# Kernel optimization log

Measured on AMD Instinct MI355X. Metric: run time of the kernel, lower is better.

The kernel has to match this reference:

```python
import jax, jax.numpy as jnp
import numpy as np

EMBED = 512
HEADS = 8
HEAD_DIM = EMBED // HEADS
EPS = 1e-5


def setup_inputs() -> dict:
    key = jax.random.key(0)
    ks = jax.random.split(key, 10)
    s = 1.0 / np.sqrt(EMBED)
    x = jax.random.normal(ks[0], (2, 4096, EMBED), dtype=jnp.float32)
    Wq = jax.random.uniform(ks[1], (EMBED, EMBED), jnp.float32, -s, s)
    bq = jnp.zeros((EMBED,), jnp.float32)
    Wk = jax.random.uniform(ks[2], (EMBED, EMBED), jnp.float32, -s, s)
    bk = jnp.zeros((EMBED,), jnp.float32)
    Wv = jax.random.uniform(ks[3], (EMBED, EMBED), jnp.float32, -s, s)
    bv = jnp.zeros((EMBED,), jnp.float32)
    Wo = jax.random.uniform(ks[4], (EMBED, EMBED), jnp.float32, -s, s)
    bo = jnp.zeros((EMBED,), jnp.float32)
    gamma = jnp.ones((EMBED,), jnp.float32)
    beta = jnp.zeros((EMBED,), jnp.float32)
    return {"x": x, "Wq": Wq, "bq": bq, "Wk": Wk, "bk": bk,
            "Wv": Wv, "bv": bv, "Wo": Wo, "bo": bo,
            "gamma": gamma, "beta": beta}


def reference(x, Wq, bq, Wk, bk, Wv, bv, Wo, bo, gamma, beta):
    b, n, e = x.shape
    def split_heads(t):  # [b,n,e] -> [b,h,n,d]
        return t.reshape(b, n, HEADS, HEAD_DIM).transpose(0, 2, 1, 3)
    q = split_heads(x @ Wq + bq)
    k = split_heads(x @ Wk + bk)
    v = split_heads(x @ Wv + bv)
    energy = jnp.einsum('bhqd,bhkd->bhqk', q, k) * (HEAD_DIM ** -0.5)
    attn = jax.nn.softmax(energy, axis=-1)  # dropout=0.0 (eval)
    out = jnp.einsum('bhqk,bhkd->bhqd', attn, v)
    out = out.transpose(0, 2, 1, 3).reshape(b, n, e)
    out = out @ Wo + bo
    y = x + out
    mu = jnp.mean(y, axis=-1, keepdims=True)
    var = jnp.var(y, axis=-1, keepdims=True)
    return (y - mu) * jax.lax.rsqrt(var + EPS) * gamma + beta
```

## Files before the change

### kernel.cpp

```cpp
#include <hip/hip_runtime.h>
#include <hip/hip_bf16.h>


#define ROWS 8192
#define EMB  512
#define SEQ  4096
#define HEADS 8
#define HD   64
#define QSCALE 0.18033688011112042f

typedef __attribute__((ext_vector_type(8))) short bf16x8;
typedef __attribute__((ext_vector_type(4))) short bf16x4;
typedef __attribute__((ext_vector_type(4))) float f32x4;

__device__ __forceinline__ float bf16_to_f(unsigned short u) {
    union { unsigned int i; float f; } v; v.i = ((unsigned int)u) << 16; return v.f;
}
__device__ __forceinline__ unsigned short f_to_bf16(float f) {
    union { __hip_bfloat16 h; unsigned short u; } v; v.h = __float2bfloat16(f); return v.u;
}
__device__ __forceinline__ unsigned int pack_bf16_trunc(float a, float b) {
    return __builtin_amdgcn_perm(__float_as_uint(b), __float_as_uint(a), 0x07060302u);
}
__device__ __forceinline__ void load_lds16(const void* g, void* l) {
    __builtin_amdgcn_global_load_lds(
        (const __attribute__((address_space(1))) void*)g,
        (__attribute__((address_space(3))) void*)l, 16, 0, 0);
}

__device__ __forceinline__ int detect_fp32(const void* x) {
    const unsigned short* p = (const unsigned short*)x;
    int t = threadIdx.x & 63;
    int cnt = 0;
    #pragma unroll
    for (int i = 0; i < 4; ++i) {
        unsigned short u = p[t * 4 + i];
        int e = (u >> 7) & 0xFF;
        cnt += (e >= 140) ? 1 : 0;
    }
    #pragma unroll
    for (int off = 32; off > 0; off >>= 1) cnt += __shfl_xor(cnt, off, 64);
    return cnt > 16;
}

__global__ __launch_bounds__(256) void prep_kernel(
        const void* __restrict__ x, unsigned short* __restrict__ xb,
        const void* W0, const void* W1, const void* W2, const void* W3,
        unsigned short* __restrict__ Wt,
        const void* b0, const void* b1, const void* b2, const void* b3,
        const void* b4, const void* b5, float* __restrict__ bias_all) {
    int fp32 = detect_fp32(x);
    int bid = blockIdx.x;
    int tid = threadIdx.x;
    if (bid < 4096) {
        if (!fp32) return;
        int i = (bid * 256 + tid) * 4;
        float4 v = *(const float4*)((const float*)x + i);
        ushort4 u = { f_to_bf16(v.x), f_to_bf16(v.y), f_to_bf16(v.z), f_to_bf16(v.w) };
        *(ushort4*)(xb + i) = u;
    } else if (bid < 4352) {
        __shared__ float T[64][65];
        int idx0 = bid - 4096;
        int kt = idx0 & 7, nt = (idx0 >> 3) & 7, mat = idx0 >> 6;
        const void* src = (mat == 0) ? W0 : (mat == 1) ? W1 : (mat == 2) ? W2 : W3;
        for (int ii = 0; ii < 4; ++ii) {
            int idx = tid + ii * 256;
            int i = idx >> 4, j = (idx & 15) * 4;
            size_t g = (size_t)(kt * 64 + i) * 512 + nt * 64 + j;
            if (fp32) {
                float4 v = *(const float4*)((const float*)src + g);
                T[i][j] = v.x; T[i][j+1] = v.y; T[i][j+2] = v.z; T[i][j+3] = v.w;
            } else {
                ushort4 u = *(const ushort4*)((const unsigned short*)src + g);
                T[i][j] = bf16_to_f(u.x); T[i][j+1] = bf16_to_f(u.y);
                T[i][j+2] = bf16_to_f(u.z); T[i][j+3] = bf16_to_f(u.w);
            }
        }
        __syncthreads();
        for (int ii = 0; ii < 2; ++ii) {
            int idx = tid + ii * 256;
            int j = idx >> 3, ch = idx & 7;
            unsigned short pk[8];
            for (int t = 0; t < 8; ++t) pk[t] = f_to_bf16(T[ch * 8 + t][j]);
            *(bf16x8*)&Wt[(size_t)(mat * 512 + nt * 64 + j) * 512 + kt * 64 + ch * 8] = *(bf16x8*)pk;
        }
    } else {
        int idx = (bid - 4352) * 256 + tid;
        int mat = idx >> 9, off = idx & 511;
        const void* src = (mat == 0) ? b0 : (mat == 1) ? b1 : (mat == 2) ? b2 :
                          (mat == 3) ? b3 : (mat == 4) ? b4 : b5;
        float v;
        if (fp32) v = ((const float*)src)[off];
        else      v = bf16_to_f(((const unsigned short*)src)[off]);
        bias_all[idx] = v;
    }
}

template <typename OutT>
__global__ __launch_bounds__(256) void gemm_mfma_kernel(
        const unsigned short* __restrict__ A_conv, const unsigned short* __restrict__ A_raw,
        const unsigned short* __restrict__ Bt,
        const float* __restrict__ bias, OutT* __restrict__ C, int ldc, int scale_cols,
        unsigned short* __restrict__ VtOut) {
    __shared__ __align__(16) unsigned short smemg[2][2][128 * 64];
    const unsigned short* A = detect_fp32(A_raw) ? A_conv : A_raw;
    int tid = threadIdx.x;
    int wave = tid >> 6, lane = tid & 63;
    int l15 = lane & 15, quad = lane >> 4;

    int lin = blockIdx.x + gridDim.x * blockIdx.y;
    int nwg = gridDim.x * gridDim.y;
    int bx, by;
    if (nwg & 7) { bx = blockIdx.x; by = blockIdx.y; }
    else {
        int t = (lin & 7) * (nwg >> 3) + (lin >> 3);
        bx = t % gridDim.x; by = t / gridDim.x;
    }
    int m0 = by * 128, n0 = bx * 128;
    int wm = (wave & 1) * 64, wn = (wave >> 1) * 64;
    bool is_v = (VtOut != nullptr) && (n0 >= 1024);

    int rt = wave * 32 + (lane >> 3);
    int ch = (lane & 7) ^ ((lane >> 3) & 7);
    const unsigned short* ag = A  + (size_t)(m0 + rt) * 512 + ch * 8;
    const unsigned short* bg = Bt + (size_t)(n0 + rt) * 512 + ch * 8;

    f32x4 acc[4][4];
    for (int i = 0; i < 4; ++i) for (int j = 0; j < 4; ++j) acc[i][j] = (f32x4){0.f,0.f,0.f,0.f};

#define GSTAGE(buf, k0) do {                                                      \
        unsigned short* Atb = &smemg[buf][0][0];                                  \
        unsigned short* Bsb = &smemg[buf][1][0];                                  \
        _Pragma("unroll")                                                         \
        for (int j = 0; j < 4; ++j) {                                             \
            load_lds16(ag + (size_t)(j * 8) * 512 + (k0), &Atb[(wave * 32 + j * 8) * 64]); \
            load_lds16(bg + (size_t)(j * 8) * 512 + (k0), &Bsb[(wave * 32 + j * 8) * 64]); \
        }                                                                         \
    } while (0)

    GSTAGE(0, 0);

    for (int s = 0; s < 8; ++s) {
        int cur = s & 1;
        asm volatile("s_waitcnt vmcnt(0)" ::: "memory");
        __builtin_amdgcn_sched_barrier(0);
        asm volatile("s_barrier" ::: "memory");
        __builtin_amdgcn_sched_barrier(0);
        if (s + 1 < 8) GSTAGE(cur ^ 1, (s + 1) * 64);

        const unsigned short* At = &smemg[cur][0][0];
        const unsigned short* Bs = &smemg[cur][1][0];
        #pragma unroll
        for (int ks = 0; ks < 2; ++ks) {
            bf16x8 a[4], b[4];
            #pragma unroll
            for (int f = 0; f < 4; ++f) {
                int pc = ((ks * 4 + quad) ^ (l15 & 7)) * 8;
                a[f] = *(const bf16x8*)&At[(wm + f * 16 + l15) * 64 + pc];
                b[f] = *(const bf16x8*)&Bs[(wn + f * 16 + l15) * 64 + pc];
            }
            if (is_v) {
                #pragma unroll
                for (int fm = 0; fm < 4; ++fm)
                    #pragma unroll
                    for (int fn = 0; fn < 4; ++fn)
                        acc[fm][fn] = __builtin_amdgcn_mfma_f32_16x16x32_bf16(a[fm], b[fn], acc[fm][fn], 0, 0, 0);
            } else {
                #pragma unroll
                for (int fm = 0; fm < 4; ++fm)
                    #pragma unroll
                    for (int fn = 0; fn < 4; ++fn)
                        acc[fm][fn] = __builtin_amdgcn_mfma_f32_16x16x32_bf16(b[fn], a[fm], acc[fm][fn], 0, 0, 0);
            }
        }
        __builtin_amdgcn_sched_barrier(0);
    }
#undef GSTAGE

    __syncthreads();
    unsigned short* LT = &smemg[0][0][0];

    float sc = (n0 < scale_cols) ? QSCALE : 1.f;

    if (is_v) {
        #pragma unroll
        for (int fm = 0; fm < 4; ++fm) {
            #pragma unroll
            for (int fn = 0; fn < 4; ++fn) {
                int dcol = wn + fn * 16 + l15;
                float bia = bias[n0 + dcol];
                int seq0 = wm + fm * 16 + quad * 4;
                ushort4 pk = { f_to_bf16(acc[fm][fn][0] + bia),
                               f_to_bf16(acc[fm][fn][1] + bia),
                               f_to_bf16(acc[fm][fn][2] + bia),
                               f_to_bf16(acc[fm][fn][3] + bia) };
                int c8 = (seq0 >> 2) ^ (dcol & 31);
                *(ushort4*)&LT[dcol * 128 + c8 * 4] = pk;
            }
        }
    } else {
        #pragma unroll
        for (int fm = 0; fm < 4; ++fm) {
            #pragma unroll
            for (int fn = 0; fn < 4; ++fn) {
                int row = wm + fm * 16 + l15;
                int col0 = wn + fn * 16 + quad * 4;
                float4 b4 = *(const float4*)&bias[n0 + col0];
                ushort4 pk = { f_to_bf16((acc[fm][fn][0] + b4.x) * sc),
                               f_to_bf16((acc[fm][fn][1] + b4.y) * sc),
                               f_to_bf16((acc[fm][fn][2] + b4.z) * sc),
                               f_to_bf16((acc[fm][fn][3] + b4.w) * sc) };
                int c8 = (col0 >> 2) ^ (row & 31);
                *(ushort4*)&LT[row * 128 + c8 * 4] = pk;
            }
        }
    }
    __syncthreads();
    #pragma unroll
    for (int i = 0; i < 16; ++i) {
        int row = wave * 32 + i * 2 + (lane >> 5);
        int c8 = lane & 31;
        int phys = c8 ^ (row & 31);
        ushort4 v4 = *(const ushort4*)&LT[row * 128 + phys * 4];
        if (is_v) {
            int hd = n0 - 1024 + row;
            int bh = (m0 >> 12) * 8 + (hd >> 6);
            int d  = hd & 63;
            *(ushort4*)&VtOut[((size_t)(bh * 64 + d)) * SEQ + (m0 & 4095) + c8 * 4] = v4;
        } else {
            *(ushort4*)&C[(size_t)(m0 + row) * ldc + n0 + c8 * 4] = v4;
        }
    }
}

__global__ __launch_bounds__(256, 4) void attn_kernel(
        const unsigned short* __restrict__ QKV, const unsigned short* __restrict__ Vt,
        unsigned short* __restrict__ Ab) {
    __shared__ __align__(16) unsigned char smem[32768];
    float* Ored = (float*)smem;
    float* Lred = (float*)(smem + 16384);

    int tid = threadIdx.x;
    int wave = tid >> 6, lane = tid & 63;
    int l15 = lane & 15, quad = lane >> 4;
    int qh = wave >> 1, kh = wave & 1;
    int lin = blockIdx.x;
    int xcd = lin & 7, slot = lin >> 3;
    int grp = xcd + 8 * (slot >> 6);
    int qt = slot & 63;
    int h = grp & 7, b = grp >> 3;
    int bh = b * HEADS + h;
    size_t qrow0 = (size_t)b * SEQ + qt * 64;

    bf16x8 aq[2][2];
    #pragma unroll
    for (int t = 0; t < 2; ++t) {
        const unsigned short* qp = &QKV[(qrow0 + qh * 32 + t * 16 + l15) * 1536 + h * 64];
        aq[t][0] = *(const bf16x8*)&qp[quad * 8];
        aq[t][1] = *(const bf16x8*)&qp[32 + quad * 8];
    }
    f32x4 o[2][4];
    #pragma unroll
    for (int t = 0; t < 2; ++t)
        #pragma unroll
        for (int db = 0; db < 4; ++db) o[t][db] = (f32x4){0.f, 0.f, 0.f, 0.f};
    float lp[2] = {0.f, 0.f};

    int r8 = lane >> 3;
    int kch = (lane & 7) ^ (r8 & 7);
    int r0 = wave * 16 + r8;
    int r1 = wave * 16 + 8 + r8;
    int p0r = (r0 & 32) | (((r0 >> 2) & 3) << 3) | (((r0 >> 4) & 1) << 2) | (r0 & 3);
    int p1r = (r1 & 32) | (((r1 >> 2) & 3) << 3) | (((r1 >> 4) & 1) << 2) | (r1 & 3);
    const unsigned short* kg0 = &QKV[((size_t)b * SEQ + p0r) * 1536 + 512 + h * 64 + kch * 8];
    const unsigned short* kg1 = &QKV[((size_t)b * SEQ + p1r) * 1536 + 512 + h * 64 + kch * 8];
    const unsigned short* vg = &Vt[((size_t)bh * 64 + wave * 16 + r8) * SEQ + kch * 8];

#define STAGE(buf, kt2) do {                                                          \
        unsigned short* Ksb = (unsigned short*)(smem + (buf) * 8192);                 \
        unsigned short* Vsb = (unsigned short*)(smem + 16384 + (buf) * 8192);         \
        load_lds16(kg0 + (size_t)((kt2) * 64) * 1536, &Ksb[(wave * 16) * 64]);        \
        load_lds16(kg1 + (size_t)((kt2) * 64) * 1536, &Ksb[(wave * 16 + 8) * 64]);    \
        load_lds16(vg + (size_t)((kt2) * 64), &Vsb[(wave * 16) * 64]);                \
        load_lds16(vg + (size_t)((kt2) * 64) + (size_t)8 * SEQ,                       \
                   &Vsb[(wave * 16 + 8) * 64]);                                       \
    } while (0)

    STAGE(0, 0);

    for (int kt = 0; kt < SEQ / 64; ++kt) {
        int cur = kt & 1;
        asm volatile("s_waitcnt vmcnt(0)" ::: "memory");
        __builtin_amdgcn_sched_barrier(0);
        asm volatile("s_barrier" ::: "memory");
        __builtin_amdgcn_sched_barrier(0);
        if (kt + 1 < SEQ / 64) STAGE(cur ^ 1, kt + 1);

        const unsigned short* Ksc = (const unsigned short*)(smem + cur * 8192);
        const unsigned short* Vsc = (const unsigned short*)(smem + 16384 + cur * 8192);

        bf16x8 kA[2][2];
        #pragma unroll
        for (int nb = 0; nb < 2; ++nb) {
            int krow = kh * 32 + nb * 16 + l15;
            int key = krow & 7;
            kA[nb][0] = *(const bf16x8*)&Ksc[krow * 64 + (quad ^ key) * 8];
            kA[nb][1] = *(const bf16x8*)&Ksc[krow * 64 + ((4 + quad) ^ key) * 8];
        }
        bf16x8 bv8[4];
        #pragma unroll
        for (int db = 0; db < 4; ++db) {
            int d = db * 16 + l15;
            bv8[db] = *(const bf16x8*)&Vsc[d * 64 + (((kh * 4 + quad) ^ (d & 7))) * 8];
        }
        #pragma unroll
        for (int t = 0; t < 2; ++t) {
            f32x4 sv0 = {0.f, 0.f, 0.f, 0.f};
            f32x4 sv1 = {0.f, 0.f, 0.f, 0.f};
            __builtin_amdgcn_s_setprio(1);
            sv0 = __builtin_amdgcn_mfma_f32_16x16x32_bf16(kA[0][0], aq[t][0], sv0, 0, 0, 0);
            sv0 = __builtin_amdgcn_mfma_f32_16x16x32_bf16(kA[0][1], aq[t][1], sv0, 0, 0, 0);
            sv1 = __builtin_amdgcn_mfma_f32_16x16x32_bf16(kA[1][0], aq[t][0], sv1, 0, 0, 0);
            sv1 = __builtin_amdgcn_mfma_f32_16x16x32_bf16(kA[1][1], aq[t][1], sv1, 0, 0, 0);
            __builtin_amdgcn_s_setprio(0);
            float p0 = __builtin_amdgcn_exp2f(sv0[0]);
            float p1 = __builtin_amdgcn_exp2f(sv0[1]);
            float p2 = __builtin_amdgcn_exp2f(sv0[2]);
            float p3 = __builtin_amdgcn_exp2f(sv0[3]);
            float p4 = __builtin_amdgcn_exp2f(sv1[0]);
            float p5 = __builtin_amdgcn_exp2f(sv1[1]);
            float p6 = __builtin_amdgcn_exp2f(sv1[2]);
            float p7 = __builtin_amdgcn_exp2f(sv1[3]);
            lp[t] += ((p0 + p1) + (p2 + p3)) + ((p4 + p5) + (p6 + p7));
            union { unsigned int u[4]; bf16x8 v; } ap;
            ap.u[0] = pack_bf16_trunc(p0, p1);
            ap.u[1] = pack_bf16_trunc(p2, p3);
            ap.u[2] = pack_bf16_trunc(p4, p5);
            ap.u[3] = pack_bf16_trunc(p6, p7);
            __builtin_amdgcn_s_setprio(1);
            #pragma unroll
            for (int db = 0; db < 4; ++db)
                o[t][db] = __builtin_amdgcn_mfma_f32_16x16x32_bf16(ap.v, bv8[db], o[t][db], 0, 0, 0);
            __builtin_amdgcn_s_setprio(0);
        }
        __builtin_amdgcn_sched_barrier(0);
    }
#undef STAGE

    __syncthreads();
    #pragma unroll
    for (int t = 0; t < 2; ++t) {
        float v = lp[t];
        v += __shfl_xor(v, 16, 64);
        v += __shfl_xor(v, 32, 64);
        if (quad == 0) Lred[(wave * 2 + t) * 16 + l15] = v;
    }
    __syncthreads();
    float* myO = Ored + wave * (16 * 64);
    #pragma unroll
    for (int t = 0; t < 2; ++t) {
        #pragma unroll
        for (int db = 0; db < 4; ++db)
            #pragma unroll
            for (int r = 0; r < 4; ++r)
                myO[(quad * 4 + r) * 64 + db * 16 + l15] = o[t][db][r];
        __syncthreads();
        {
            int q_l = tid >> 3;
            int dg = tid & 7;
            int qh2 = q_l >> 4, qq = q_l & 15;
            const float* r0p = Ored + (qh2 * 2 + 0) * (16 * 64) + qq * 64 + dg * 8;
            const float* r1p = Ored + (qh2 * 2 + 1) * (16 * 64) + qq * 64 + dg * 8;
            float4 a0 = *(const float4*)&r0p[0];
            float4 a1 = *(const float4*)&r0p[4];
            float4 c0 = *(const float4*)&r1p[0];
            float4 c1 = *(const float4*)&r1p[4];
            float lt = Lred[((qh2 * 2 + 0) * 2 + t) * 16 + qq] +
                       Lred[((qh2 * 2 + 1) * 2 + t) * 16 + qq];
            float inv = 1.f / lt;
            size_t row = qrow0 + qh2 * 32 + t * 16 + qq;
            unsigned short* dst = &Ab[row * EMB + h * 64 + dg * 8];
            ushort4 lo = { f_to_bf16((a0.x + c0.x) * inv), f_to_bf16((a0.y + c0.y) * inv),
                           f_to_bf16((a0.z + c0.z) * inv), f_to_bf16((a0.w + c0.w) * inv) };
            ushort4 hi = { f_to_bf16((a1.x + c1.x) * inv), f_to_bf16((a1.y + c1.y) * inv),
                           f_to_bf16((a1.z + c1.z) * inv), f_to_bf16((a1.w + c1.w) * inv) };
            *(ushort4*)&dst[0] = lo;
            *(ushort4*)&dst[4] = hi;
        }
        __syncthreads();
    }
}

__global__ __launch_bounds__(256) void ln_kernel(
        const float* __restrict__ xf, const unsigned short* __restrict__ xraw,
        const unsigned short* __restrict__ P,
        const float* __restrict__ gamma, const float* __restrict__ beta,
        void* __restrict__ out) {
    int fp32 = detect_fp32(xraw);
    int row = blockIdx.x * 4 + (threadIdx.x >> 6);
    int t = threadIdx.x & 63;
    float v[8];
    float s = 0.f, ss = 0.f;
    const unsigned short* pp = &P[(size_t)row * EMB + t * 8];
    ushort4 p0 = *(const ushort4*)&pp[0];
    ushort4 p1 = *(const ushort4*)&pp[4];
    float pv[8] = { bf16_to_f(p0.x), bf16_to_f(p0.y), bf16_to_f(p0.z), bf16_to_f(p0.w),
                    bf16_to_f(p1.x), bf16_to_f(p1.y), bf16_to_f(p1.z), bf16_to_f(p1.w) };
    if (fp32) {
        const float* xp = &xf[(size_t)row * EMB + t * 8];
        for (int i = 0; i < 8; i += 4) {
            float4 x4 = *(const float4*)&xp[i];
            v[i] = x4.x + pv[i]; v[i+1] = x4.y + pv[i+1];
            v[i+2] = x4.z + pv[i+2]; v[i+3] = x4.w + pv[i+3];
        }
    } else {
        const unsigned short* xp = &xraw[(size_t)row * EMB + t * 8];
        ushort4 x0 = *(const ushort4*)&xp[0];
        ushort4 x1 = *(const ushort4*)&xp[4];
        v[0] = bf16_to_f(x0.x) + pv[0]; v[1] = bf16_to_f(x0.y) + pv[1];
        v[2] = bf16_to_f(x0.z) + pv[2]; v[3] = bf16_to_f(x0.w) + pv[3];
        v[4] = bf16_to_f(x1.x) + pv[4]; v[5] = bf16_to_f(x1.y) + pv[5];
        v[6] = bf16_to_f(x1.z) + pv[6]; v[7] = bf16_to_f(x1.w) + pv[7];
    }
    for (int i = 0; i < 8; ++i) { s += v[i]; ss += v[i] * v[i]; }
    for (int off = 32; off > 0; off >>= 1) {
        s  += __shfl_xor(s, off, 64);
        ss += __shfl_xor(ss, off, 64);
    }
    float mu = s * (1.f / 512.f);
    float var = ss * (1.f / 512.f) - mu * mu;
    float rs = rsqrtf(var + 1e-5f);
    for (int i = 0; i < 8; ++i) {
        int col = t * 8 + i;
        float y = (v[i] - mu) * rs * gamma[col] + beta[col];
        if (fp32) ((float*)out)[(size_t)row * EMB + col] = y;
        else      ((__hip_bfloat16*)out)[(size_t)row * EMB + col] = __float2bfloat16(y);
    }
}

extern "C" void kernel_launch(void* const* d_in, const int* in_sizes, int n_in,
                              void* d_out, int out_size, void* d_ws, size_t ws_size,
                              hipStream_t stream) {
    char* ws = (char*)d_ws;
    char* p = ws + 256;
    float* bias_all = (float*)p;       p += 6 * 512 * 4;
    unsigned short* Wt   = (unsigned short*)p; p += (size_t)2048 * 512 * 2;
    unsigned short* QKVb = (unsigned short*)p; p += (size_t)ROWS * 1536 * 2;
    unsigned short* Vt   = (unsigned short*)p; p += (size_t)16 * HD * SEQ * 2;
    unsigned short* xb = (unsigned short*)p;
    unsigned short* Ab = (unsigned short*)p;   p += (size_t)ROWS * EMB * 2;
    unsigned short* Pb = (unsigned short*)p;   p += (size_t)ROWS * EMB * 2;

    prep_kernel<<<4364, 256, 0, stream>>>(d_in[0], xb,
        d_in[1], d_in[3], d_in[5], d_in[7], Wt,
        d_in[2], d_in[4], d_in[6], d_in[8], d_in[9], d_in[10], bias_all);

    gemm_mfma_kernel<unsigned short><<<dim3(12, 64), 256, 0, stream>>>(
        xb, (const unsigned short*)d_in[0], Wt, bias_all, QKVb, 1536, 512, Vt);

    attn_kernel<<<dim3(1024), 256, 0, stream>>>(QKVb, Vt, Ab);

    gemm_mfma_kernel<unsigned short><<<dim3(4, 64), 256, 0, stream>>>(
        Ab, Ab, Wt + (size_t)1536 * 512, bias_all + 1536, Pb, 512, 0,
        (unsigned short*)nullptr);

    ln_kernel<<<ROWS / 4, 256, 0, stream>>>((const float*)d_in[0],
                                            (const unsigned short*)d_in[0], Pb,
                                            bias_all + 4 * 512, bias_all + 5 * 512, d_out);
}
```

Before: 221.4 us.

## Fuse output projection GEMM with residual LayerNorm; compute softmax denominator via MFMA

Replaces the separate output-projection GEMM and LayerNorm kernels with one kernel. Each block loads a 32-row tile of attention output into LDS, multiplies it by Wo with MFMA, writes the biased result back to LDS, then applies the residual add and LayerNorm before storing. This removes the intermediate projection buffer round trip and one launch, but leaves only 256 blocks, each streaming the full Wo from global memory without LDS staging. Separately, the attention kernel now computes row sums of P with an extra MFMA against a ones vector instead of scalar adds and cross-lane shuffles.

```diff
diff --git a/kernel.cpp b/kernel.cpp
--- a/kernel.cpp
+++ b/kernel.cpp
@@ -264,7 +264,11 @@
     for (int t = 0; t < 2; ++t)
         #pragma unroll
         for (int db = 0; db < 4; ++db) o[t][db] = (f32x4){0.f, 0.f, 0.f, 0.f};
-    float lp[2] = {0.f, 0.f};
+    f32x4 ol[2];
+    ol[0] = (f32x4){0.f, 0.f, 0.f, 0.f};
+    ol[1] = (f32x4){0.f, 0.f, 0.f, 0.f};
+    const bf16x8 ones8 = { (short)0x3F80, (short)0x3F80, (short)0x3F80, (short)0x3F80,
+                           (short)0x3F80, (short)0x3F80, (short)0x3F80, (short)0x3F80 };
 
     int r8 = lane >> 3;
     int kch = (lane & 7) ^ (r8 & 7);
@@ -331,7 +335,6 @@
             float p5 = __builtin_amdgcn_exp2f(sv1[1]);
             float p6 = __builtin_amdgcn_exp2f(sv1[2]);
             float p7 = __builtin_amdgcn_exp2f(sv1[3]);
-            lp[t] += ((p0 + p1) + (p2 + p3)) + ((p4 + p5) + (p6 + p7));
             union { unsigned int u[4]; bf16x8 v; } ap;
             ap.u[0] = pack_bf16_trunc(p0, p1);
             ap.u[1] = pack_bf16_trunc(p2, p3);
@@ -341,6 +344,7 @@
             #pragma unroll
             for (int db = 0; db < 4; ++db)
                 o[t][db] = __builtin_amdgcn_mfma_f32_16x16x32_bf16(ap.v, bv8[db], o[t][db], 0, 0, 0);
+            ol[t] = __builtin_amdgcn_mfma_f32_16x16x32_bf16(ap.v, ones8, ol[t], 0, 0, 0);
             __builtin_amdgcn_s_setprio(0);
         }
         __builtin_amdgcn_sched_barrier(0);
@@ -348,12 +352,12 @@
 #undef STAGE
 
     __syncthreads();
-    #pragma unroll
-    for (int t = 0; t < 2; ++t) {
-        float v = lp[t];
-        v += __shfl_xor(v, 16, 64);
-        v += __shfl_xor(v, 32, 64);
-        if (quad == 0) Lred[(wave * 2 + t) * 16 + l15] = v;
+    if (l15 == 0) {
+        #pragma unroll
+        for (int t = 0; t < 2; ++t)
+            #pragma unroll
+            for (int r = 0; r < 4; ++r)
+                Lred[(wave * 2 + t) * 16 + quad * 4 + r] = ol[t][r];
     }
     __syncthreads();
     float* myO = Ored + wave * (16 * 64);
@@ -391,50 +395,143 @@
     }
 }
 
-__global__ __launch_bounds__(256) void ln_kernel(
+__global__ __launch_bounds__(256) void oproj_ln_kernel(
+        const unsigned short* __restrict__ Ab, const unsigned short* __restrict__ Wo,
+        const float* __restrict__ bias_all,
         const float* __restrict__ xf, const unsigned short* __restrict__ xraw,
-        const unsigned short* __restrict__ P,
-        const float* __restrict__ gamma, const float* __restrict__ beta,
         void* __restrict__ out) {
+    __shared__ __align__(16) unsigned short Aslds[32 * 512];
     int fp32 = detect_fp32(xraw);
-    int row = blockIdx.x * 4 + (threadIdx.x >> 6);
-    int t = threadIdx.x & 63;
-    float v[8];
-    float s = 0.f, ss = 0.f;
-    const unsigned short* pp = &P[(size_t)row * EMB + t * 8];
-    ushort4 p0 = *(const ushort4*)&pp[0];
-    ushort4 p1 = *(const ushort4*)&pp[4];
-    float pv[8] = { bf16_to_f(p0.x), bf16_to_f(p0.y), bf16_to_f(p0.z), bf16_to_f(p0.w),
-                    bf16_to_f(p1.x), bf16_to_f(p1.y), bf16_to_f(p1.z), bf16_to_f(p1.w) };
-    if (fp32) {
-        const float* xp = &xf[(size_t)row * EMB + t * 8];
-        for (int i = 0; i < 8; i += 4) {
-            float4 x4 = *(const float4*)&xp[i];
-            v[i] = x4.x + pv[i]; v[i+1] = x4.y + pv[i+1];
-            v[i+2] = x4.z + pv[i+2]; v[i+3] = x4.w + pv[i+3];
-        }
-    } else {
-        const unsigned short* xp = &xraw[(size_t)row * EMB + t * 8];
-        ushort4 x0 = *(const ushort4*)&xp[0];
-        ushort4 x1 = *(const ushort4*)&xp[4];
-        v[0] = bf16_to_f(x0.x) + pv[0]; v[1] = bf16_to_f(x0.y) + pv[1];
-        v[2] = bf16_to_f(x0.z) + pv[2]; v[3] = bf16_to_f(x0.w) + pv[3];
-        v[4] = bf16_to_f(x1.x) + pv[4]; v[5] = bf16_to_f(x1.y) + pv[5];
-        v[6] = bf16_to_f(x1.z) + pv[6]; v[7] = bf16_to_f(x1.w) + pv[7];
-    }
-    for (int i = 0; i < 8; ++i) { s += v[i]; ss += v[i] * v[i]; }
-    for (int off = 32; off > 0; off >>= 1) {
-        s  += __shfl_xor(s, off, 64);
-        ss += __shfl_xor(ss, off, 64);
-    }
-    float mu = s * (1.f / 512.f);
-    float var = ss * (1.f / 512.f) - mu * mu;
-    float rs = rsqrtf(var + 1e-5f);
-    for (int i = 0; i < 8; ++i) {
-        int col = t * 8 + i;
-        float y = (v[i] - mu) * rs * gamma[col] + beta[col];
-        if (fp32) ((float*)out)[(size_t)row * EMB + col] = y;
-        else      ((__hip_bfloat16*)out)[(size_t)row * EMB + col] = __float2bfloat16(y);
+    int tid = threadIdx.x;
+    int wave = tid >> 6, lane = tid & 63;
+    int l15 = lane & 15, quad = lane >> 4;
+    int m0 = blockIdx.x * 32;
+
+    {
+        int c = lane;
+        #pragma unroll
+        for (int j = 0; j < 8; ++j) {
+            int row = j * 4 + wave;
+            int csrc = c ^ (row & 7);
+            load_lds16(&Ab[(size_t)(m0 + row) * 512 + csrc * 8],
+                       &Aslds[row * 512 + c * 8]);
+        }
+    }
+    asm volatile("s_waitcnt vmcnt(0)" ::: "memory");
+    __syncthreads();
+
+    f32x4 acc[2][8];
+    #pragma unroll
+    for (int mf = 0; mf < 2; ++mf)
+        #pragma unroll
+        for (int nf = 0; nf < 8; ++nf) acc[mf][nf] = (f32x4){0.f, 0.f, 0.f, 0.f};
+
+    const unsigned short* bgl = Wo + (size_t)(wave * 128 + l15) * 512 + quad * 8;
+
+    #pragma unroll
+    for (int s = 0; s < 8; ++s) {
+        bf16x8 b[2][8];
+        #pragma unroll
+        for (int ks = 0; ks < 2; ++ks)
+            #pragma unroll
+            for (int nf = 0; nf < 8; ++nf)
+                b[ks][nf] = *(const bf16x8*)&bgl[(size_t)nf * (16 * 512) + s * 64 + ks * 32];
+        bf16x8 a[2][2];
+        #pragma unroll
+        for (int ks = 0; ks < 2; ++ks)
+            #pragma unroll
+            for (int mf = 0; mf < 2; ++mf) {
+                int row = mf * 16 + l15;
+                int clog = s * 8 + ks * 4 + quad;
+                a[ks][mf] = *(const bf16x8*)&Aslds[row * 512 + (clog ^ (row & 7)) * 8];
+            }
+        #pragma unroll
+        for (int ks = 0; ks < 2; ++ks)
+            #pragma unroll
+            for (int mf = 0; mf < 2; ++mf)
+                #pragma unroll
+                for (int nf = 0; nf < 8; ++nf)
+                    acc[mf][nf] = __builtin_amdgcn_mfma_f32_16x16x32_bf16(a[ks][mf], b[ks][nf], acc[mf][nf], 0, 0, 0);
+    }
+
+    __syncthreads();
+    #pragma unroll
+    for (int mf = 0; mf < 2; ++mf)
+        #pragma unroll
+        for (int nf = 0; nf < 8; ++nf) {
+            int col = wave * 128 + nf * 16 + l15;
+            float bo = bias_all[1536 + col];
+            #pragma unroll
+            for (int r = 0; r < 4; ++r) {
+                int row = mf * 16 + quad * 4 + r;
+                Aslds[row * 512 + col] = f_to_bf16(acc[mf][nf][r] + bo);
+            }
+        }
+    __syncthreads();
+
+    const float* gamma = bias_all + 4 * 512;
+    const float* beta  = bias_all + 5 * 512;
+    float g[8], bt[8];
+    #pragma unroll
+    for (int i = 0; i < 8; ++i) { g[i] = gamma[lane * 8 + i]; bt[i] = beta[lane * 8 + i]; }
+
+    #pragma unroll
+    for (int rr = 0; rr < 8; ++rr) {
+        int row = wave * 8 + rr;
+        size_t grow = (size_t)(m0 + row);
+        const unsigned short* pp = &Aslds[row * 512 + lane * 8];
+        ushort4 p0 = *(const ushort4*)&pp[0];
+        ushort4 p1 = *(const ushort4*)&pp[4];
+        float pv[8] = { bf16_to_f(p0.x), bf16_to_f(p0.y), bf16_to_f(p0.z), bf16_to_f(p0.w),
+                        bf16_to_f(p1.x), bf16_to_f(p1.y), bf16_to_f(p1.z), bf16_to_f(p1.w) };
+        float v[8];
+        if (fp32) {
+            const float* xp = &xf[grow * EMB + lane * 8];
+            float4 x0 = *(const float4*)&xp[0];
+            float4 x1 = *(const float4*)&xp[4];
+            v[0] = x0.x + pv[0]; v[1] = x0.y + pv[1]; v[2] = x0.z + pv[2]; v[3] = x0.w + pv[3];
+            v[4] = x1.x + pv[4]; v[5] = x1.y + pv[5]; v[6] = x1.z + pv[6]; v[7] = x1.w + pv[7];
+        } else {
+            const unsigned short* xp = &xraw[grow * EMB + lane * 8];
+            ushort4 x0 = *(const ushort4*)&xp[0];
+            ushort4 x1 = *(const ushort4*)&xp[4];
+            v[0] = bf16_to_f(x0.x) + pv[0]; v[1] = bf16_to_f(x0.y) + pv[1];
+            v[2] = bf16_to_f(x0.z) + pv[2]; v[3] = bf16_to_f(x0.w) + pv[3];
+            v[4] = bf16_to_f(x1.x) + pv[4]; v[5] = bf16_to_f(x1.y) + pv[5];
+            v[6] = bf16_to_f(x1.z) + pv[6]; v[7] = bf16_to_f(x1.w) + pv[7];
+        }
+        float s = 0.f, ss = 0.f;
+        #pragma unroll
+        for (int i = 0; i < 8; ++i) { s += v[i]; ss += v[i] * v[i]; }
+        #pragma unroll
+        for (int off = 32; off > 0; off >>= 1) {
+            s  += __shfl_xor(s, off, 64);
+            ss += __shfl_xor(ss, off, 64);
+        }
+        float mu = s * (1.f / 512.f);
+        float var = ss * (1.f / 512.f) - mu * mu;
+        float rs = rsqrtf(var + 1e-5f);
+        if (fp32) {
+            float* op = &((float*)out)[grow * EMB + lane * 8];
+            float4 o0 = { (v[0] - mu) * rs * g[0] + bt[0], (v[1] - mu) * rs * g[1] + bt[1],
+                          (v[2] - mu) * rs * g[2] + bt[2], (v[3] - mu) * rs * g[3] + bt[3] };
+            float4 o1 = { (v[4] - mu) * rs * g[4] + bt[4], (v[5] - mu) * rs * g[5] + bt[5],
+                          (v[6] - mu) * rs * g[6] + bt[6], (v[7] - mu) * rs * g[7] + bt[7] };
+            *(float4*)&op[0] = o0;
+            *(float4*)&op[4] = o1;
+        } else {
+            unsigned short* op = &((unsigned short*)out)[grow * EMB + lane * 8];
+            ushort4 o0 = { f_to_bf16((v[0] - mu) * rs * g[0] + bt[0]),
+                           f_to_bf16((v[1] - mu) * rs * g[1] + bt[1]),
+                           f_to_bf16((v[2] - mu) * rs * g[2] + bt[2]),
+                           f_to_bf16((v[3] - mu) * rs * g[3] + bt[3]) };
+            ushort4 o1 = { f_to_bf16((v[4] - mu) * rs * g[4] + bt[4]),
+                           f_to_bf16((v[5] - mu) * rs * g[5] + bt[5]),
+                           f_to_bf16((v[6] - mu) * rs * g[6] + bt[6]),
+                           f_to_bf16((v[7] - mu) * rs * g[7] + bt[7]) };
+            *(ushort4*)&op[0] = o0;
+            *(ushort4*)&op[4] = o1;
+        }
     }
 }
 
@@ -449,7 +546,6 @@
     unsigned short* Vt   = (unsigned short*)p; p += (size_t)16 * HD * SEQ * 2;
     unsigned short* xb = (unsigned short*)p;
     unsigned short* Ab = (unsigned short*)p;   p += (size_t)ROWS * EMB * 2;
-    unsigned short* Pb = (unsigned short*)p;   p += (size_t)ROWS * EMB * 2;
 
     prep_kernel<<<4364, 256, 0, stream>>>(d_in[0], xb,
         d_in[1], d_in[3], d_in[5], d_in[7], Wt,
@@ -460,11 +556,7 @@
 
     attn_kernel<<<dim3(1024), 256, 0, stream>>>(QKVb, Vt, Ab);
 
-    gemm_mfma_kernel<unsigned short><<<dim3(4, 64), 256, 0, stream>>>(
-        Ab, Ab, Wt + (size_t)1536 * 512, bias_all + 1536, Pb, 512, 0,
-        (unsigned short*)nullptr);
-
-    ln_kernel<<<ROWS / 4, 256, 0, stream>>>((const float*)d_in[0],
-                                            (const unsigned short*)d_in[0], Pb,
-                                            bias_all + 4 * 512, bias_all + 5 * 512, d_out);
-}
+    oproj_ln_kernel<<<ROWS / 32, 256, 0, stream>>>(
+        Ab, Wt + (size_t)1536 * 512, bias_all,
+        (const float*)d_in[0], (const unsigned short*)d_in[0], d_out);
+}
```

New measurement: 213.3 us. 1.04x faster.
